# Performance work log

Hardware: AMD Instinct MI355X
Metric: run time of the kernel (lower is better)

## Reference

```python
import jax, jax.numpy as jnp
import numpy as np

VOXEL = 64          # voxel_size
MAX_DEPTH = 10.0    # depth_range[1]
SMIN, SMAX = -2.0, 2.0  # spatial_range


def setup_inputs() -> dict:
    key = jax.random.key(0)
    B, H, W = 32, 512, 512
    rgbd = jax.random.uniform(key, (B, 4, H, W), dtype=jnp.float32)
    # scale depth channel to a realistic metric range [0, 8) so that a
    # meaningful fraction of back-projected points falls inside [-2, 2]
    rgbd = rgbd.at[:, 3].multiply(8.0)
    return {"rgbd": rgbd}


def reference(rgbd):
    B, C, H, W = rgbd.shape
    V = VOXEL
    dt = rgbd.dtype

    rgb = jnp.transpose(rgbd[:, :3], (0, 2, 3, 1))   # [B,H,W,3]
    d = rgbd[:, 3]                                   # [B,H,W]

    # intrinsics is None -> default pinhole
    fx = fy = min(H, W) / 2.0
    cx, cy = W / 2.0, H / 2.0

    u = jnp.arange(W, dtype=dt)[None, None, :]       # column index (x)
    v = jnp.arange(H, dtype=dt)[None, :, None]       # row index (y)

    # depth -> pointcloud (per pixel)
    x = (u - cx) * d / fx
    y = (v - cy) * d / fy
    pts = jnp.stack([x, y, d], axis=-1)              # [B,H,W,3]

    depth_valid = (d > 0) & (d < MAX_DEPTH) & jnp.isfinite(d)

    # pointcloud -> voxel coordinates
    coords = jnp.round((pts - SMIN) / (SMAX - SMIN) * (V - 1)).astype(jnp.int32)
    in_range = jnp.all((coords >= 0) & (coords < V), axis=-1)
    mask = depth_valid & in_range                    # [B,H,W]
    coords = jnp.clip(coords, 0, V - 1)

    b_idx = jnp.arange(B, dtype=jnp.int32)[:, None, None]
    lin = ((b_idx * V + coords[..., 0]) * V + coords[..., 1]) * V + coords[..., 2]
    lin = lin.reshape(-1)                            # [B*H*W]
    w = mask.astype(dt).reshape(-1)                  # [B*H*W]

    nseg = B * V * V * V
    count = jax.ops.segment_sum(w, lin, num_segments=nseg)                 # [B*V^3]
    csum = jax.ops.segment_sum(rgb.reshape(-1, 3) * w[:, None], lin,
                               num_segments=nseg)                          # [B*V^3,3]

    occ = (count > 0).astype(dt)                                           # occupancy = 1 where any point lands
    color = jnp.where(count[:, None] > 0,
                      csum / jnp.maximum(count, 1.0)[:, None],
                      jnp.zeros((), dt))                                   # mean color per occupied voxel

    occ = occ.reshape(B, V, V, V)
    color = color.reshape(B, V, V, V, 3).transpose(0, 4, 1, 2, 3)
    return jnp.concatenate([occ[:, None], color], axis=1)  # [B,4,V,V,V]
```

## Files before the change

kernel.cpp:

```cpp
#include <hip/hip_runtime.h>
#include <math.h>


constexpr int V = 64;
constexpr int V3 = V * V * V;
constexpr int Wd = 512, Hd = 512;
constexpr int NPIX = Wd * Hd;
constexpr int NBUCKET = 32 * 256;
constexpr unsigned CAPQ = 3456;
constexpr float CQ = 16384.0f;
constexpr int PPB = 2048;
constexpr int CHUNKS = NPIX / PPB;

typedef float f4 __attribute__((ext_vector_type(4)));

__device__ __forceinline__ bool unproject(int w, int h, float d,
                                          int& ix, int& iy, int& iz) {
    if (!(d > 0.0f) || !(d < 10.0f) || !isfinite(d)) return false;
    const float fx = 256.0f, cx = 256.0f, cy = 256.0f;
    float x = (((float)w - cx) * d) / fx;
    float y = (((float)h - cy) * d) / fx;
    float tx = rintf(((x + 2.0f) * 0.25f) * 63.0f);
    float ty = rintf(((y + 2.0f) * 0.25f) * 63.0f);
    float tz = rintf(((d + 2.0f) * 0.25f) * 63.0f);
    ix = (int)tx; iy = (int)ty; iz = (int)tz;
    return !(ix < 0 || ix >= V || iy < 0 || iy >= V ||
             iz < 0 || iz >= V);
}

__global__ void dtv_cursor_init(unsigned* __restrict__ cursor) {
    int i = blockIdx.x * blockDim.x + threadIdx.x;
    cursor[i] = (unsigned)i * CAPQ;
}

__global__ void __launch_bounds__(256)
dtv_append4(const float* __restrict__ rgbd,
            unsigned* __restrict__ cursor,
            unsigned long long* __restrict__ entries) {
    int blk = blockIdx.x;
    int b = blk >> 7, chunk = blk & (CHUNKS - 1), t = threadIdx.x;

    __shared__ unsigned lcnt[256];
    __shared__ unsigned lpre[256];
    __shared__ unsigned labs[256];
    __shared__ unsigned wtot[4];
    __shared__ unsigned long long stage[PPB];

    lcnt[t] = 0;
    __syncthreads();

    const float* bb = rgbd + (size_t)b * 4 * NPIX;
    const f4* r4 = (const f4*)(bb) + chunk * (PPB / 4);
    const f4* g4 = (const f4*)(bb + (size_t)NPIX) + chunk * (PPB / 4);
    const f4* b4 = (const f4*)(bb + (size_t)2 * NPIX) + chunk * (PPB / 4);
    const f4* d4 = (const f4*)(bb + (size_t)3 * NPIX) + chunk * (PPB / 4);
    int pbase = chunk * PPB;

    f4 dv[2], rv[2], gv[2], bv[2];
#pragma unroll
    for (int i = 0; i < 2; ++i) dv[i] = __builtin_nontemporal_load(&d4[t + i * 256]);
#pragma unroll
    for (int i = 0; i < 2; ++i) {
        rv[i] = __builtin_nontemporal_load(&r4[t + i * 256]);
        gv[i] = __builtin_nontemporal_load(&g4[t + i * 256]);
        bv[i] = __builtin_nontemporal_load(&b4[t + i * 256]);
    }

    unsigned meta[8];
#pragma unroll
    for (int i = 0; i < 2; ++i) {
        int p0 = pbase + 4 * (t + i * 256);
#pragma unroll
        for (int j = 0; j < 4; ++j) {
            float d = dv[i][j];
            int pix = p0 + j;
            int h = pix >> 9, w = pix & (Wd - 1);
            int ix, iy, iz;
            if (unproject(w, h, d, ix, iy, iz)) {
                unsigned bin = ((unsigned)ix << 2) | ((unsigned)iy >> 4);
                unsigned off = atomicAdd(&lcnt[bin], 1u);
                meta[i * 4 + j] = (bin << 24) | ((unsigned)iy << 18) |
                                  ((unsigned)iz << 12) | off;
            } else {
                meta[i * 4 + j] = 0xFFFFFFFFu;
            }
        }
    }
    __syncthreads();

    {
        int w = t >> 6, lane = t & 63;
        unsigned c = lcnt[t];
        unsigned s = c;
#pragma unroll
        for (int off = 1; off < 64; off <<= 1) {
            unsigned v = __shfl_up(s, off, 64);
            if (lane >= off) s += v;
        }
        if (lane == 63) wtot[w] = s;
        __syncthreads();
        unsigned woff = 0;
#pragma unroll
        for (int k = 0; k < 3; ++k)
            if (k < w) woff += wtot[k];
        lpre[t] = woff + s - c;
        labs[t] = c ? atomicAdd(&cursor[b * 256 + t], c) : 0u;
    }
    __syncthreads();

#pragma unroll
    for (int i = 0; i < 2; ++i) {
#pragma unroll
        for (int j = 0; j < 4; ++j) {
            unsigned m = meta[i * 4 + j];
            if (m == 0xFFFFFFFFu) continue;
            unsigned bin = m >> 24, iy = (m >> 18) & 63u, iz = (m >> 12) & 63u;
            unsigned ix = bin >> 2;
            unsigned off = m & 0xFFFu;
            float r  = rv[i][j];
            float g  = gv[i][j];
            float bl = bv[i][j];
            unsigned long long r14 = (unsigned long long)(unsigned)rintf(r  * CQ);
            unsigned long long g14 = (unsigned long long)(unsigned)rintf(g  * CQ);
            unsigned long long b14 = (unsigned long long)(unsigned)rintf(bl * CQ);
            unsigned slot = lpre[bin] + off;
            stage[slot] = ((unsigned long long)ix << 57) |
                          ((unsigned long long)iy << 51) |
                          ((unsigned long long)iz << 45) |
                          (r14 << 30) | (g14 << 15) | b14;
        }
    }
    __syncthreads();

    unsigned total = lpre[255] + lcnt[255];
    for (unsigned e = t; e < total; e += 256) {
        unsigned long long ent = stage[e];
        unsigned bin = (unsigned)(ent >> 55) & 255u;
        unsigned pos = labs[bin] + (e - lpre[bin]);
        unsigned kk4 = (unsigned)(b * 256) + bin;
        if (pos < (kk4 + 1) * CAPQ)
            entries[(size_t)pos] = ent;
    }
}

__global__ void __launch_bounds__(256)
dtv_reduce4(const ulonglong2* __restrict__ entries2,
            const unsigned* __restrict__ cursor,
            float* __restrict__ out) {
    int bq = blockIdx.x;
    unsigned rank = (unsigned)bq >> 7;
    int ix = (rank & 1u) ? (31 - (int)(rank >> 1)) : (32 + (int)(rank >> 1));
    int b  = (bq >> 2) & 31;
    unsigned quad = (unsigned)(bq & 3);
    int kk4 = b * 256 + ix * 4 + (int)quad;
    int t = threadIdx.x;

    __shared__ unsigned long long ldsA[1024];
    __shared__ unsigned long long ldsB[1024];

    unsigned basew = (unsigned)kk4 * CAPQ;
    unsigned cnt = cursor[kk4] - basew;
    if (cnt > CAPQ) cnt = CAPQ;
    unsigned npair = cnt >> 1;
    size_t base2 = (size_t)kk4 * (CAPQ / 2);

    ulonglong2 e2;
    if (t < (int)npair) e2 = entries2[base2 + t];

    ulonglong2* zA = (ulonglong2*)ldsA;
    ulonglong2* zB = (ulonglong2*)ldsB;
#pragma unroll
    for (int i = 0; i < 2; ++i) {
        zA[t + i * 256] = ulonglong2{0ULL, 0ULL};
        zB[t + i * 256] = ulonglong2{0ULL, 0ULL};
    }
    __syncthreads();

    auto accum = [&](unsigned long long p) {
        unsigned iy4 = (unsigned)(p >> 51) & 15u;
        unsigned iz  = (unsigned)(p >> 45) & 63u;
        unsigned v = iy4 * 64u + iz;
        atomicAdd(&ldsA[v], (1ULL << 32) | ((p >> 30) & 0x7FFFULL));
        atomicAdd(&ldsB[v], (((p >> 15) & 0x7FFFULL) << 32) | (p & 0x7FFFULL));
    };

    for (unsigned j = t; j < npair; j += 256) {
        ulonglong2 cur = e2;
        unsigned jn = j + 256;
        if (jn < npair) e2 = entries2[base2 + jn];
        accum(cur.x);
        accum(cur.y);
    }
    if ((cnt & 1u) && t == 0) {
        const unsigned long long* e1 = (const unsigned long long*)entries2;
        accum(e1[(size_t)basew + cnt - 1]);
    }
    __syncthreads();

    float* p0 = out + (size_t)b * 4 * V3 + (size_t)ix * 4096 + quad * 1024;
    int v0 = t * 4;
    f4 o0, o1, o2, o3;
#pragma unroll
    for (int j = 0; j < 4; ++j) {
        unsigned long long A = ldsA[v0 + j], Bw = ldsB[v0 + j];
        unsigned c = (unsigned)(A >> 32);
        float occ = 0.0f, r = 0.0f, g = 0.0f, bl = 0.0f;
        if (c) {
            float inv = 1.0f / (CQ * (float)c);
            occ = 1.0f;
            r  = (float)(unsigned)(A  & 0xFFFFFFFFULL) * inv;
            g  = (float)(unsigned)(Bw >> 32)            * inv;
            bl = (float)(unsigned)(Bw & 0xFFFFFFFFULL)  * inv;
        }
        o0[j] = occ; o1[j] = r; o2[j] = g; o3[j] = bl;
    }
    __builtin_nontemporal_store(o0, (f4*)(p0) + t);
    __builtin_nontemporal_store(o1, (f4*)(p0 + (size_t)V3) + t);
    __builtin_nontemporal_store(o2, (f4*)(p0 + (size_t)2 * V3) + t);
    __builtin_nontemporal_store(o3, (f4*)(p0 + (size_t)3 * V3) + t);
}

__global__ void dtv_scatter_f32(const float* __restrict__ rgbd,
                                float* __restrict__ acc) {
    int idx = blockIdx.x * blockDim.x + threadIdx.x;
    int b   = idx >> 18;
    int pix = idx & (NPIX - 1);
    int h   = pix >> 9;
    int w   = pix & (Wd - 1);
    const float* base = rgbd + (size_t)b * 4 * NPIX;
    float d = base[(size_t)3 * NPIX + pix];
    int ix, iy, iz;
    if (!unproject(w, h, d, ix, iy, iz)) return;
    float r  = base[pix];
    float g  = base[(size_t)NPIX + pix];
    float bl = base[(size_t)2 * NPIX + pix];
    float* ob = acc + (size_t)b * 4 * V3;
    int vlin = (ix * V + iy) * V + iz;
    atomicAdd(ob + vlin, 1.0f);
    atomicAdd(ob + (size_t)V3 + vlin, r);
    atomicAdd(ob + (size_t)2 * V3 + vlin, g);
    atomicAdd(ob + (size_t)3 * V3 + vlin, bl);
}

__global__ void dtv_finalize_f32(float* __restrict__ out) {
    int idx = blockIdx.x * blockDim.x + threadIdx.x;
    int b    = idx >> 18;
    int vlin = idx & (V3 - 1);
    float* p = out + (size_t)b * 4 * V3;
    float c  = p[vlin];
    float r  = p[(size_t)V3 + vlin];
    float g  = p[(size_t)2 * V3 + vlin];
    float bl = p[(size_t)3 * V3 + vlin];
    bool occ = (c > 0.0f);
    p[vlin]                  = occ ? 1.0f : 0.0f;
    p[(size_t)V3 + vlin]     = occ ? (r / c)  : 0.0f;
    p[(size_t)2 * V3 + vlin] = occ ? (g / c)  : 0.0f;
    p[(size_t)3 * V3 + vlin] = occ ? (bl / c) : 0.0f;
}

extern "C" void kernel_launch(void* const* d_in, const int* in_sizes, int n_in,
                              void* d_out, int out_size, void* d_ws, size_t ws_size,
                              hipStream_t stream) {
    const float* rgbd = (const float*)d_in[0];
    float* out = (float*)d_out;
    const int B = in_sizes[0] / (4 * NPIX);

    size_t need = 32768 + (size_t)NBUCKET * CAPQ * sizeof(unsigned long long);

    if (B == 32 && ws_size >= need) {
        unsigned* cursor = (unsigned*)d_ws;
        unsigned long long* entries =
            (unsigned long long*)((char*)d_ws + 32768);
        dtv_cursor_init<<<NBUCKET / 256, 256, 0, stream>>>(cursor);
        dtv_append4    <<<B * CHUNKS, 256, 0, stream>>>(rgbd, cursor, entries);
        dtv_reduce4    <<<NBUCKET, 256, 0, stream>>>((const ulonglong2*)entries,
                                                     cursor, out);
    } else {
        (void)hipMemsetAsync(d_out, 0, (size_t)out_size * sizeof(float), stream);
        int total_pix = B * NPIX;
        int total_vox = B * V3;
        dtv_scatter_f32 <<<(total_pix + 255) / 256, 256, 0, stream>>>(rgbd, out);
        dtv_finalize_f32<<<(total_vox + 255) / 256, 256, 0, stream>>>(out);
    }
}
```

Measured before the change: 242.7 us.

## Store compact pixel-index keys in buckets and gather RGB in reduce kernel

The append kernel no longer reads RGB or builds 64-bit packed entries staged through shared memory. It now writes 32-bit keys (iy, iz, pixel index) directly to the global buckets without the LDS prefix-sum staging. The reduce kernel gathers r,g,b from the input image by pixel index and quantizes them there. This halves intermediate bucket traffic and removes a staging pass, but global writes become uncoalesced and RGB reads in reduce become scattered gathers.

```diff
diff --git a/kernel.cpp b/kernel.cpp
--- a/kernel.cpp
+++ b/kernel.cpp
@@ -36,7 +36,7 @@
 __global__ void __launch_bounds__(256)
 dtv_append4(const float* __restrict__ rgbd,
             unsigned* __restrict__ cursor,
-            unsigned long long* __restrict__ entries) {
+            unsigned* __restrict__ entries) {
     int blk = blockIdx.x;
     int b = blk >> 7, chunk = blk & (CHUNKS - 1), t = threadIdx.x;
 
@@ -44,27 +44,17 @@
     __shared__ unsigned lpre[256];
     __shared__ unsigned labs[256];
     __shared__ unsigned wtot[4];
-    __shared__ unsigned long long stage[PPB];
 
     lcnt[t] = 0;
     __syncthreads();
 
     const float* bb = rgbd + (size_t)b * 4 * NPIX;
-    const f4* r4 = (const f4*)(bb) + chunk * (PPB / 4);
-    const f4* g4 = (const f4*)(bb + (size_t)NPIX) + chunk * (PPB / 4);
-    const f4* b4 = (const f4*)(bb + (size_t)2 * NPIX) + chunk * (PPB / 4);
     const f4* d4 = (const f4*)(bb + (size_t)3 * NPIX) + chunk * (PPB / 4);
     int pbase = chunk * PPB;
 
-    f4 dv[2], rv[2], gv[2], bv[2];
+    f4 dv[2];
 #pragma unroll
     for (int i = 0; i < 2; ++i) dv[i] = __builtin_nontemporal_load(&d4[t + i * 256]);
-#pragma unroll
-    for (int i = 0; i < 2; ++i) {
-        rv[i] = __builtin_nontemporal_load(&r4[t + i * 256]);
-        gv[i] = __builtin_nontemporal_load(&g4[t + i * 256]);
-        bv[i] = __builtin_nontemporal_load(&b4[t + i * 256]);
-    }
 
     unsigned meta[8];
 #pragma unroll
@@ -88,64 +78,35 @@
     }
     __syncthreads();
 
-    {
-        int w = t >> 6, lane = t & 63;
+    if (t < 256) {
         unsigned c = lcnt[t];
-        unsigned s = c;
-#pragma unroll
-        for (int off = 1; off < 64; off <<= 1) {
-            unsigned v = __shfl_up(s, off, 64);
-            if (lane >= off) s += v;
-        }
-        if (lane == 63) wtot[w] = s;
-        __syncthreads();
-        unsigned woff = 0;
-#pragma unroll
-        for (int k = 0; k < 3; ++k)
-            if (k < w) woff += wtot[k];
-        lpre[t] = woff + s - c;
         labs[t] = c ? atomicAdd(&cursor[b * 256 + t], c) : 0u;
     }
     __syncthreads();
+    (void)lpre; (void)wtot;
 
 #pragma unroll
     for (int i = 0; i < 2; ++i) {
+        int p0 = pbase + 4 * (t + i * 256);
 #pragma unroll
         for (int j = 0; j < 4; ++j) {
             unsigned m = meta[i * 4 + j];
             if (m == 0xFFFFFFFFu) continue;
             unsigned bin = m >> 24, iy = (m >> 18) & 63u, iz = (m >> 12) & 63u;
-            unsigned ix = bin >> 2;
             unsigned off = m & 0xFFFu;
-            float r  = rv[i][j];
-            float g  = gv[i][j];
-            float bl = bv[i][j];
-            unsigned long long r14 = (unsigned long long)(unsigned)rintf(r  * CQ);
-            unsigned long long g14 = (unsigned long long)(unsigned)rintf(g  * CQ);
-            unsigned long long b14 = (unsigned long long)(unsigned)rintf(bl * CQ);
-            unsigned slot = lpre[bin] + off;
-            stage[slot] = ((unsigned long long)ix << 57) |
-                          ((unsigned long long)iy << 51) |
-                          ((unsigned long long)iz << 45) |
-                          (r14 << 30) | (g14 << 15) | b14;
+            unsigned pix = (unsigned)(p0 + j);
+            unsigned kk4 = (unsigned)(b * 256) + bin;
+            unsigned pos = labs[bin] + off;
+            if (pos < (kk4 + 1) * CAPQ)
+                entries[(size_t)pos] = (iy << 24) | (iz << 18) | pix;
         }
     }
-    __syncthreads();
-
-    unsigned total = lpre[255] + lcnt[255];
-    for (unsigned e = t; e < total; e += 256) {
-        unsigned long long ent = stage[e];
-        unsigned bin = (unsigned)(ent >> 55) & 255u;
-        unsigned pos = labs[bin] + (e - lpre[bin]);
-        unsigned kk4 = (unsigned)(b * 256) + bin;
-        if (pos < (kk4 + 1) * CAPQ)
-            entries[(size_t)pos] = ent;
-    }
 }
 
 __global__ void __launch_bounds__(256)
-dtv_reduce4(const ulonglong2* __restrict__ entries2,
+dtv_reduce4(const unsigned* __restrict__ entries,
             const unsigned* __restrict__ cursor,
+            const float* __restrict__ rgbd,
             float* __restrict__ out) {
     int bq = blockIdx.x;
     unsigned rank = (unsigned)bq >> 7;
@@ -161,11 +122,9 @@
     unsigned basew = (unsigned)kk4 * CAPQ;
     unsigned cnt = cursor[kk4] - basew;
     if (cnt > CAPQ) cnt = CAPQ;
-    unsigned npair = cnt >> 1;
-    size_t base2 = (size_t)kk4 * (CAPQ / 2);
-
-    ulonglong2 e2;
-    if (t < (int)npair) e2 = entries2[base2 + t];
+
+    unsigned key0 = 0;
+    if (t < (int)cnt) key0 = entries[(size_t)basew + t];
 
     ulonglong2* zA = (ulonglong2*)ldsA;
     ulonglong2* zB = (ulonglong2*)ldsB;
@@ -176,24 +135,22 @@
     }
     __syncthreads();
 
-    auto accum = [&](unsigned long long p) {
-        unsigned iy4 = (unsigned)(p >> 51) & 15u;
-        unsigned iz  = (unsigned)(p >> 45) & 63u;
+    const float* bb = rgbd + (size_t)b * 4 * NPIX;
+
+    for (unsigned j = t; j < cnt; j += 256) {
+        unsigned key = (j == (unsigned)t) ? key0 : entries[(size_t)basew + j];
+        unsigned pix = key & 0x3FFFFu;
+        float r  = bb[pix];
+        float g  = bb[(size_t)NPIX + pix];
+        float bl = bb[(size_t)2 * NPIX + pix];
+        unsigned iy4 = (key >> 24) & 15u;
+        unsigned iz  = (key >> 18) & 63u;
         unsigned v = iy4 * 64u + iz;
-        atomicAdd(&ldsA[v], (1ULL << 32) | ((p >> 30) & 0x7FFFULL));
-        atomicAdd(&ldsB[v], (((p >> 15) & 0x7FFFULL) << 32) | (p & 0x7FFFULL));
-    };
-
-    for (unsigned j = t; j < npair; j += 256) {
-        ulonglong2 cur = e2;
-        unsigned jn = j + 256;
-        if (jn < npair) e2 = entries2[base2 + jn];
-        accum(cur.x);
-        accum(cur.y);
-    }
-    if ((cnt & 1u) && t == 0) {
-        const unsigned long long* e1 = (const unsigned long long*)entries2;
-        accum(e1[(size_t)basew + cnt - 1]);
+        unsigned long long r14 = (unsigned long long)(unsigned)rintf(r  * CQ);
+        unsigned long long g14 = (unsigned long long)(unsigned)rintf(g  * CQ);
+        unsigned long long b14 = (unsigned long long)(unsigned)rintf(bl * CQ);
+        atomicAdd(&ldsA[v], (1ULL << 32) | r14);
+        atomicAdd(&ldsB[v], (g14 << 32) | b14);
     }
     __syncthreads();
 
@@ -265,16 +222,14 @@
     float* out = (float*)d_out;
     const int B = in_sizes[0] / (4 * NPIX);
 
-    size_t need = 32768 + (size_t)NBUCKET * CAPQ * sizeof(unsigned long long);
+    size_t need = 32768 + (size_t)NBUCKET * CAPQ * sizeof(unsigned);
 
     if (B == 32 && ws_size >= need) {
         unsigned* cursor = (unsigned*)d_ws;
-        unsigned long long* entries =
-            (unsigned long long*)((char*)d_ws + 32768);
+        unsigned* entries = (unsigned*)((char*)d_ws + 32768);
         dtv_cursor_init<<<NBUCKET / 256, 256, 0, stream>>>(cursor);
         dtv_append4    <<<B * CHUNKS, 256, 0, stream>>>(rgbd, cursor, entries);
-        dtv_reduce4    <<<NBUCKET, 256, 0, stream>>>((const ulonglong2*)entries,
-                                                     cursor, out);
+        dtv_reduce4    <<<NBUCKET, 256, 0, stream>>>(entries, cursor, rgbd, out);
     } else {
         (void)hipMemsetAsync(d_out, 0, (size_t)out_size * sizeof(float), stream);
         int total_pix = B * NPIX;
```

Result: slower. 303.5 us (+25.1%).
